# Kernel optimization log

Hardware: AMD Instinct MI355X
Metric: run time of the kernel (lower is better)

## Reference

```python
import jax, jax.numpy as jnp
import numpy as np

N_NODES = 100000
N_EDGES = 3200000
N_GRAPHS = 64
NEG_SLOPE = 0.2


def mish(x):
    return x * jnp.tanh(jax.nn.softplus(x))


def gat_layer(x, src, dst, W, b, a_src, a_dst, heads, out_ch, n_nodes):
    # h: [N, H, C]
    h = (x @ W).reshape(n_nodes, heads, out_ch)
    alpha_s = jnp.sum(h * a_src[None], axis=-1)  # [N, H]
    alpha_d = jnp.sum(h * a_dst[None], axis=-1)  # [N, H]
    e = jax.nn.leaky_relu(alpha_s[src] + alpha_d[dst], NEG_SLOPE)  # [E, H]
    # scatter-softmax over incoming edges of each destination node
    emax = jax.ops.segment_max(e, dst, num_segments=n_nodes)  # [N, H]
    ee = jnp.exp(e - emax[dst])
    den = jax.ops.segment_sum(ee, dst, num_segments=n_nodes)
    alpha = ee / (den[dst] + 1e-16)  # [E, H]
    msg = h[src] * alpha[..., None]  # [E, H, C]
    out = jax.ops.segment_sum(msg, dst, num_segments=n_nodes)
    return out.reshape(n_nodes, heads * out_ch) + b


def setup_inputs() -> dict:
    key = jax.random.key(0)
    ks = jax.random.split(key, 10)
    x = jax.random.normal(ks[0], (N_NODES, 128), dtype=jnp.float32)
    edge_index = jax.random.randint(ks[1], (2, N_EDGES), 0, N_NODES, dtype=jnp.int64)
    batch = jnp.sort(jax.random.randint(ks[2], (N_NODES,), 0, N_GRAPHS, dtype=jnp.int64))
    s1 = 1.0 / np.sqrt(128.0)
    s2 = 1.0 / np.sqrt(16.0)
    return {
        "x": x,
        "edge_index": edge_index,
        "batch": batch,
        "W1": jax.random.normal(ks[3], (128, 16), dtype=jnp.float32) * s1,
        "b1": jnp.zeros((16,), dtype=jnp.float32),
        "a_src1": jax.random.normal(ks[4], (4, 4), dtype=jnp.float32) * 0.5,
        "a_dst1": jax.random.normal(ks[5], (4, 4), dtype=jnp.float32) * 0.5,
        "W2": jax.random.normal(ks[6], (16, 32), dtype=jnp.float32) * s2,
        "b2": jnp.zeros((32,), dtype=jnp.float32),
        "a_src2": jax.random.normal(ks[7], (1, 32), dtype=jnp.float32) * 0.5,
        "a_dst2": jax.random.normal(ks[8], (1, 32), dtype=jnp.float32) * 0.5,
    }


def reference(x, edge_index, batch, W1, b1, a_src1, a_dst1, W2, b2, a_src2, a_dst2):
    n = x.shape[0]
    # PyG GATConv default add_self_loops=True
    loop = jnp.arange(n, dtype=edge_index.dtype)
    src = jnp.concatenate([edge_index[0], loop])
    dst = jnp.concatenate([edge_index[1], loop])
    h = mish(gat_layer(x, src, dst, W1, b1, a_src1, a_dst1, heads=4, out_ch=4, n_nodes=n))
    h = mish(gat_layer(h, src, dst, W2, b2, a_src2, a_dst2, heads=1, out_ch=32, n_nodes=n))
    # global_mean_pool
    sums = jax.ops.segment_sum(h, batch, num_segments=N_GRAPHS)
    cnts = jax.ops.segment_sum(jnp.ones((n,), h.dtype), batch, num_segments=N_GRAPHS)
    return sums / jnp.maximum(cnts, 1.0)[:, None]
```

## Files before the change

kernel.cpp:

```cpp
#include <hip/hip_runtime.h>
#include <hip/hip_fp16.h>
#include <math.h>

#define NEG_SLOPE 0.2f
#define GB 192
#define SB 320
#define CHMAX 11264
#define CAP 5120
#define CAPH 2560

typedef _Float16 half2v __attribute__((ext_vector_type(2)));
typedef _Float16 half4v __attribute__((ext_vector_type(4)));

__device__ __forceinline__ float mishf(float x) {
    if (x > 15.f) return x;
    float ex = __expf(x);
    float y = 1.f + ex;
    float y2 = y * y;
    return x * (y2 - 1.f) / (y2 + 1.f);
}

__device__ __forceinline__ float lw(float e) {
    return __expf(fmaxf(e, NEG_SLOPE * e));
}

__device__ __forceinline__ float hdot2a(half2v a, half2v b, float c) {
#if __has_builtin(__builtin_amdgcn_fdot2)
    return __builtin_amdgcn_fdot2(a, b, c, false);
#else
    return (float)a.x * (float)b.x + (float)a.y * (float)b.y + c;
#endif
}

__global__ __launch_bounds__(1024) void front_kernel(
        const float* __restrict__ x, const float* __restrict__ W1,
        const float* __restrict__ a_dst,
        const float* __restrict__ W2, const float* __restrict__ as2,
        const float* __restrict__ ad2,
        _Float16* __restrict__ hpre1h, float* __restrict__ addst,
        float* __restrict__ vs, float* __restrict__ vd,
        const int* __restrict__ src, const int* __restrict__ dst,
        int E, int Etot, int CH, int NB, int N, int NT,
        int* __restrict__ cursor, int* __restrict__ pairs) {
    __shared__ __attribute__((aligned(16))) char smem[63824];
    int tid = threadIdx.x;
    if (blockIdx.x < GB) {
        float* Wlt = (float*)smem;
        float* xs  = Wlt + 16 * 132;
        if (blockIdx.x == 0 && tid < 16) {
            float ps = 0.f, pd = 0.f;
            #pragma unroll
            for (int c = 0; c < 32; c++) {
                float w = W2[tid * 32 + c];
                ps += w * as2[c];
                pd += w * ad2[c];
            }
            vs[tid] = ps; vd[tid] = pd;
        }
        for (int i = tid; i < 2048; i += 1024) Wlt[(i & 15) * 132 + (i >> 4)] = W1[i];
        int nl = tid >> 4, ch = tid & 15;
        for (int t = blockIdx.x; t < NT; t += GB) {
            int nodebase = t * 64;
            int nvalid = min(64, N - nodebase);
            __syncthreads();
            const float4* x4 = (const float4*)(x + (size_t)nodebase * 128);
            #pragma unroll
            for (int u = 0; u < 2; u++) {
                int i = tid + (u << 10);
                int tnl = i >> 5;
                if (tnl < nvalid) {
                    float4 v = x4[i];
                    int k = (i & 31) * 4;
                    float* dp = &xs[tnl * 132 + k];
                    dp[0] = v.x; dp[1] = v.y; dp[2] = v.z; dp[3] = v.w;
                }
            }
            __syncthreads();
            if (nl < nvalid) {
                const float4* xr4 = (const float4*)&xs[nl * 132];
                const float4* wr4 = (const float4*)&Wlt[ch * 132];
                float acc = 0.f;
                #pragma unroll
                for (int k4 = 0; k4 < 32; k4++) {
                    float4 xv = xr4[k4];
                    float4 wv = wr4[k4];
                    acc += xv.x * wv.x + xv.y * wv.y + xv.z * wv.z + xv.w * wv.w;
                }
                int node = nodebase + nl;
                hpre1h[node * 16 + ch] = (_Float16)acc;
                float pd = acc * a_dst[ch];
                pd += __shfl_xor(pd, 1); pd += __shfl_xor(pd, 2);
                if ((ch & 3) == 0) addst[node * 4 + (ch >> 2)] = pd;
            }
        }
    } else {
        int nb2 = 2 * NB;
        int* A    = (int*)smem;
        int* Boff = A + nb2;
        int* C    = Boff + nb2;
        int* buf  = C + nb2;
        int blk = blockIdx.x - GB;
        for (int b = tid; b < nb2; b += 1024) A[b] = 0;
        __syncthreads();
        int ibeg = blk * CH, iend = min((blk + 1) * CH, Etot);
        int cdv[11], cs[11];
        #pragma unroll
        for (int u = 0; u < 11; u++) {
            int i = ibeg + tid + (u << 10);
            int d = -1, s = 0;
            if (i < iend) {
                if (i < E) { d = dst[i]; s = src[i]; } else { d = i - E; s = d; }
                atomicAdd(&A[d >> 6], 1);
            }
            cdv[u] = d; cs[u] = s;
        }
        for (int i = ibeg + CHMAX + tid; i < iend; i += 1024) {
            int d, s;
            if (i < E) { d = dst[i]; s = src[i]; } else { d = i - E; s = d; }
            int f = d >> 6;
            int pos = atomicAdd(&cursor[f], 1);
            pos = pos < CAPH ? pos : CAPH - 1;
            size_t addr = (size_t)(f >> 1) * CAP + ((f & 1) ? (CAP - 1 - pos) : pos);
            pairs[addr] = s | ((d & 63) << 17);
        }
        __syncthreads();
        for (int b = tid; b < nb2; b += 1024) Boff[b] = A[b];
        __syncthreads();
        for (int o = 1; o < nb2; o <<= 1) {
            int i1 = tid, i2 = tid + 1024;
            int v1 = 0, v2 = 0;
            if (i1 < nb2 && i1 >= o) v1 = Boff[i1 - o];
            if (i2 < nb2 && i2 >= o) v2 = Boff[i2 - o];
            __syncthreads();
            if (i1 < nb2) Boff[i1] += v1;
            if (i2 < nb2) Boff[i2] += v2;
            __syncthreads();
        }
        for (int b = tid; b < nb2; b += 1024) {
            int cnt = A[b];
            Boff[b] -= cnt;
            C[b] = cnt ? atomicAdd(&cursor[b], cnt) : 0;
        }
        __syncthreads();
        for (int b = tid; b < nb2; b += 1024) A[b] = 0;
        __syncthreads();
        #pragma unroll
        for (int u = 0; u < 11; u++) {
            int d = cdv[u];
            if (d < 0) continue;
            int f = d >> 6;
            int r = atomicAdd(&A[f], 1);
            buf[Boff[f] + r] = cs[u] | ((d & 63) << 17);
        }
        __syncthreads();
        int total = iend - ibeg;
        if (total > CHMAX) total = CHMAX;
        if (total < 0) total = 0;
        for (int j = tid; j < total; j += 1024) {
            int lo = 0, hi = nb2 - 1;
            while (lo < hi) {
                int mid = (lo + hi + 1) >> 1;
                if (Boff[mid] <= j) lo = mid; else hi = mid - 1;
            }
            int f = lo;
            int pos = C[f] + (j - Boff[f]);
            pos = pos < CAPH ? pos : CAPH - 1;
            size_t addr = (size_t)(f >> 1) * CAP + ((f & 1) ? (CAP - 1 - pos) : pos);
            pairs[addr] = buf[j];
        }
    }
}

__global__ __launch_bounds__(256) void csragg1_kernel(
        const int* __restrict__ pairs, const int* __restrict__ btotal,
        int NB, int N,
        int* __restrict__ ssorted, int* __restrict__ rs, int* __restrict__ re,
        const float* __restrict__ a_src1, const float* __restrict__ addst,
        const _Float16* __restrict__ hpre1h, const float* __restrict__ b1,
        const float* __restrict__ vs, const float* __restrict__ vd,
        _Float16* __restrict__ hpost1h,
        float* __restrict__ as2n, float* __restrict__ ad2n) {
    __shared__ int deg[64];
    __shared__ int s[64];
    __shared__ int cur[64];
    __shared__ __attribute__((aligned(16))) int lds_sorted[CAPH];
    int tid = threadIdx.x, bh = blockIdx.x;
    int B = bh >> 1, half = bh & 1;
    int nb0 = (B << 7) + (half << 6);
    int cnt_nodes = min(64, N - nb0);
    int c = min(btotal[bh], CAPH);
    int rbase = B * CAP + (half ? CAP - c : 0);
    if (tid < 64) deg[tid] = 0;
    __syncthreads();
    for (int j = tid; j < c; j += 256)
        atomicAdd(&deg[(pairs[rbase + j] >> 17) & 63], 1);
    __syncthreads();
    if (tid < 64) s[tid] = deg[tid];
    __syncthreads();
    for (int o = 1; o < 64; o <<= 1) {
        int v = 0;
        if (tid < 64 && tid >= o) v = s[tid - o];
        __syncthreads();
        if (tid < 64) s[tid] += v;
        __syncthreads();
    }
    if (tid < 64) {
        int ex = s[tid] - deg[tid];
        cur[tid] = ex;
        if (tid < cnt_nodes) {
            rs[nb0 + tid] = bh * CAPH + ex;
            re[nb0 + tid] = bh * CAPH + ex + deg[tid];
        }
    }
    __syncthreads();
    for (int j = tid; j < c; j += 256) {
        int p = pairs[rbase + j];
        int pos = atomicAdd(&cur[(p >> 17) & 63], 1);
        lds_sorted[pos < CAPH ? pos : CAPH - 1] = p & 0x1FFFF;
    }
    __syncthreads();

    {
        int t4 = c >> 2;
        const int4* ls4 = (const int4*)lds_sorted;
        int4* gs4 = (int4*)(ssorted + (size_t)bh * CAPH);
        for (int j = tid; j < t4; j += 256) gs4[j] = ls4[j];
        for (int j = (t4 << 2) + tid; j < c; j += 256)
            ssorted[(size_t)bh * CAPH + j] = lds_sorted[j];
    }

    int wave = tid >> 6;
    int lane = tid & 63;
    int head = lane & 3, er = lane >> 2;
    int c0 = head * 4;
    half2v w01, w23;
    w01.x = (_Float16)a_src1[c0];     w01.y = (_Float16)a_src1[c0 + 1];
    w23.x = (_Float16)a_src1[c0 + 2]; w23.y = (_Float16)a_src1[c0 + 3];
    for (int r = 0; r < 16; r++) {
        int ln = (wave << 4) + r;
        if (ln >= cnt_nodes) break;
        int node = nb0 + ln;
        int end = cur[ln];
        int start = end - deg[ln];
        float adh = addst[node * 4 + head];
        float den = 0.f, a0 = 0.f, a1 = 0.f, a2 = 0.f, a3 = 0.f;
        int last = end - 1;
        int jb = start;
        for (; jb + 16 <= end; jb += 16) {
            int s0 = lds_sorted[jb + er];
            half4v h = *(const half4v*)(hpre1h + (size_t)s0 * 16 + c0);
            half2v hlo = __builtin_shufflevector(h, h, 0, 1);
            half2v hhi = __builtin_shufflevector(h, h, 2, 3);
            float p = hdot2a(hlo, w01, hdot2a(hhi, w23, 0.f));
            float w = lw(p + adh);
            den += w;
            a0 += (float)h.x * w; a1 += (float)h.y * w;
            a2 += (float)h.z * w; a3 += (float)h.w * w;
        }
        if (jb < end) {
            int j0 = jb + er;
            int k0 = (j0 <= last) ? j0 : last;
            int s0 = lds_sorted[k0];
            half4v h = *(const half4v*)(hpre1h + (size_t)s0 * 16 + c0);
            half2v hlo = __builtin_shufflevector(h, h, 0, 1);
            half2v hhi = __builtin_shufflevector(h, h, 2, 3);
            float p = hdot2a(hlo, w01, hdot2a(hhi, w23, 0.f));
            float w = (j0 <= last) ? lw(p + adh) : 0.f;
            den += w;
            a0 += (float)h.x * w; a1 += (float)h.y * w;
            a2 += (float)h.z * w; a3 += (float)h.w * w;
        }
        a0 += __shfl_xor(a0, 4);  a1 += __shfl_xor(a1, 4);  a2 += __shfl_xor(a2, 4);  a3 += __shfl_xor(a3, 4);  den += __shfl_xor(den, 4);
        a0 += __shfl_xor(a0, 8);  a1 += __shfl_xor(a1, 8);  a2 += __shfl_xor(a2, 8);  a3 += __shfl_xor(a3, 8);  den += __shfl_xor(den, 8);
        a0 += __shfl_xor(a0, 16); a1 += __shfl_xor(a1, 16); a2 += __shfl_xor(a2, 16); a3 += __shfl_xor(a3, 16); den += __shfl_xor(den, 16);
        a0 += __shfl_xor(a0, 32); a1 += __shfl_xor(a1, 32); a2 += __shfl_xor(a2, 32); a3 += __shfl_xor(a3, 32); den += __shfl_xor(den, 32);
        if (er == 0) {
            float inv = 1.f / (den + 1e-16f);
            float o0 = mishf(a0 * inv + b1[c0]);
            float o1 = mishf(a1 * inv + b1[c0 + 1]);
            float o2 = mishf(a2 * inv + b1[c0 + 2]);
            float o3 = mishf(a3 * inv + b1[c0 + 3]);
            half4v oh;
            oh.x = (_Float16)o0; oh.y = (_Float16)o1;
            oh.z = (_Float16)o2; oh.w = (_Float16)o3;
            *(half4v*)(hpost1h + (size_t)node * 16 + c0) = oh;
            float ps = o0 * vs[c0] + o1 * vs[c0 + 1] + o2 * vs[c0 + 2] + o3 * vs[c0 + 3];
            float pd = o0 * vd[c0] + o1 * vd[c0 + 1] + o2 * vd[c0 + 2] + o3 * vd[c0 + 3];
            ps += __shfl_xor(ps, 1); pd += __shfl_xor(pd, 1);
            ps += __shfl_xor(ps, 2); pd += __shfl_xor(pd, 2);
            if (head == 0) { as2n[node] = ps; ad2n[node] = pd; }
        }
    }
}

__global__ void agg2_kernel(const int* __restrict__ rs, const int* __restrict__ re,
                            const int* __restrict__ ssorted,
                            const float* __restrict__ as2n, const float* __restrict__ ad2n,
                            const _Float16* __restrict__ hpost1h,
                            float* __restrict__ agg16, float* __restrict__ denv, int N) {
    int wave = threadIdx.x >> 6;
    int lane = threadIdx.x & 63;
    int node = blockIdx.x * 4 + wave;
    if (node >= N) return;
    int start = rs[node], end = re[node];
    int q = lane & 3, er = lane >> 2;
    int c0 = q * 4;
    float adh = ad2n[node];
    const _Float16* hb = hpost1h + c0;
    float den = 0.f, a0 = 0.f, a1 = 0.f, a2 = 0.f, a3 = 0.f;
    int last = end - 1;
    int jb = start;
    for (; jb + 16 <= end; jb += 16) {
        int s0 = __builtin_nontemporal_load(ssorted + jb + er);
        float w = lw(as2n[s0] + adh);
        half4v h = *(const half4v*)(hb + (size_t)s0 * 16);
        den += w;
        a0 += (float)h.x * w; a1 += (float)h.y * w;
        a2 += (float)h.z * w; a3 += (float)h.w * w;
    }
    if (jb < end) {
        int j0 = jb + er;
        int k0 = (j0 <= last) ? j0 : last;
        int s0 = __builtin_nontemporal_load(ssorted + k0);
        float w = (j0 <= last) ? lw(as2n[s0] + adh) : 0.f;
        half4v h = *(const half4v*)(hb + (size_t)s0 * 16);
        den += w;
        a0 += (float)h.x * w; a1 += (float)h.y * w;
        a2 += (float)h.z * w; a3 += (float)h.w * w;
    }
    a0 += __shfl_xor(a0, 4);  a1 += __shfl_xor(a1, 4);  a2 += __shfl_xor(a2, 4);  a3 += __shfl_xor(a3, 4);  den += __shfl_xor(den, 4);
    a0 += __shfl_xor(a0, 8);  a1 += __shfl_xor(a1, 8);  a2 += __shfl_xor(a2, 8);  a3 += __shfl_xor(a3, 8);  den += __shfl_xor(den, 8);
    a0 += __shfl_xor(a0, 16); a1 += __shfl_xor(a1, 16); a2 += __shfl_xor(a2, 16); a3 += __shfl_xor(a3, 16); den += __shfl_xor(den, 16);
    a0 += __shfl_xor(a0, 32); a1 += __shfl_xor(a1, 32); a2 += __shfl_xor(a2, 32); a3 += __shfl_xor(a3, 32); den += __shfl_xor(den, 32);
    if (er == 0) {
        float4 o; o.x = a0; o.y = a1; o.z = a2; o.w = a3;
        *(float4*)(agg16 + (size_t)node * 16 + c0) = o;
        if (q == 0) denv[node] = den;
    }
}

__global__ void post2pool_kernel(const float* __restrict__ agg16, const float* __restrict__ denv,
                                 const float* __restrict__ W2, const float* __restrict__ b2,
                                 const int* __restrict__ batch,
                                 float* __restrict__ pool, float* __restrict__ cnt, int N) {
    __shared__ float Wl[16 * 32];
    int tid = threadIdx.x;
    for (int i = tid; i < 512; i += 256) Wl[i] = W2[i];
    __syncthreads();
    int r = tid >> 5, ch = tid & 31;
    float bc = b2[ch];
    int base = blockIdx.x * 128;
    int cur = -1;
    float sum = 0.f, c = 0.f;
    for (int it = 0; it < 16; it++) {
        int n = base + it * 8 + r;
        if (n >= N) break;
        int g = batch[n];
        if (g != cur) {
            if (cur >= 0) {
                atomicAdd(&pool[cur * 32 + ch], sum);
                if (ch == 0) atomicAdd(&cnt[cur], c);
            }
            cur = g; sum = 0.f; c = 0.f;
        }
        const float* ar = agg16 + (size_t)n * 16;
        float acc = 0.f;
        #pragma unroll
        for (int k = 0; k < 16; k++) acc += ar[k] * Wl[k * 32 + ch];
        float val = mishf(acc / (denv[n] + 1e-16f) + bc);
        sum += val;
        c += 1.f;
    }
    if (cur >= 0) {
        atomicAdd(&pool[cur * 32 + ch], sum);
        if (ch == 0) atomicAdd(&cnt[cur], c);
    }
}

__global__ void fin_kernel(const float* __restrict__ pool, const float* __restrict__ cnt,
                           float* __restrict__ out, int NG) {
    int i = blockIdx.x * blockDim.x + threadIdx.x;
    if (i >= NG * 32) return;
    out[i] = pool[i] / fmaxf(cnt[i >> 5], 1.0f);
}

extern "C" void kernel_launch(void* const* d_in, const int* in_sizes, int n_in,
                              void* d_out, int out_size, void* d_ws, size_t ws_size,
                              hipStream_t stream) {
    const float* x   = (const float*)d_in[0];
    const int* eidx  = (const int*)d_in[1];
    const int* batch = (const int*)d_in[2];
    const float* W1  = (const float*)d_in[3];
    const float* b1  = (const float*)d_in[4];
    const float* as1 = (const float*)d_in[5];
    const float* ad1 = (const float*)d_in[6];
    const float* W2  = (const float*)d_in[7];
    const float* b2  = (const float*)d_in[8];
    const float* as2 = (const float*)d_in[9];
    const float* ad2 = (const float*)d_in[10];
    float* out = (float*)d_out;

    int N = in_sizes[0] / 128;
    int E = in_sizes[1] / 2;
    int Etot = E + N;
    int NG = out_size / 32;
    const int* esrc = eidx;
    const int* edst = eidx + E;

    int NB = (N + 127) >> 7;
    int NBH = NB * 2;
    int NT = (N + 63) >> 6;
    int CH = (Etot + SB - 1) / SB;

    char* p = (char*)d_ws;
    auto alloc = [&](size_t nbytes) {
        p = (char*)(((uintptr_t)p + 15) & ~(uintptr_t)15);
        void* r = (void*)p; p += nbytes; return r;
    };
    int* pairs        = (int*)alloc((size_t)NB * CAP * 4);
    int* ssorted      = (int*)alloc((size_t)NBH * CAPH * 4);
    int* rs           = (int*)alloc((size_t)N * 4);
    int* re           = (int*)alloc((size_t)N * 4);
    int* cursor       = (int*)alloc((size_t)NBH * 4);
    _Float16* hpre1h  = (_Float16*)alloc((size_t)N * 16 * 2);
    _Float16* hpost1h = (_Float16*)alloc((size_t)N * 16 * 2);
    float* addst1  = (float*)alloc((size_t)N * 4 * 4);
    float* as2n    = (float*)alloc((size_t)N * 4);
    float* ad2n    = (float*)alloc((size_t)N * 4);
    float* agg16   = (float*)alloc((size_t)N * 16 * 4);
    float* denv    = (float*)alloc((size_t)N * 4);
    float* vs      = (float*)alloc(16 * 4);
    float* vd      = (float*)alloc(16 * 4);
    float* pool    = (float*)alloc((size_t)NG * 32 * 4);
    float* cnt     = (float*)alloc((size_t)NG * 4);

    hipMemsetAsync(cursor, 0, (size_t)NBH * 4, stream);
    hipMemsetAsync(pool, 0, (size_t)NG * 32 * 4, stream);
    hipMemsetAsync(cnt, 0, (size_t)NG * 4, stream);

    front_kernel<<<GB + SB, 1024, 0, stream>>>(x, W1, ad1, W2, as2, ad2,
                                               hpre1h, addst1, vs, vd,
                                               esrc, edst, E, Etot, CH, NB, N, NT,
                                               cursor, pairs);
    csragg1_kernel<<<NBH, 256, 0, stream>>>(pairs, cursor, NB, N,
                                            ssorted, rs, re, as1, addst1, hpre1h,
                                            b1, vs, vd, hpost1h, as2n, ad2n);
    agg2_kernel<<<(N + 3) / 4, 256, 0, stream>>>(rs, re, ssorted, as2n, ad2n, hpost1h,
                                                 agg16, denv, N);
    post2pool_kernel<<<(N + 127) / 128, 256, 0, stream>>>(agg16, denv, W2, b2, batch,
                                                          pool, cnt, N);
    fin_kernel<<<(NG * 32 + 255) / 256, 256, 0, stream>>>(pool, cnt, out, NG);
}
```

Baseline: 332.9 us.

## Fuse CSR build, both aggregations and pooling into one cooperative kernel

Replaces the csragg1, agg2 and post2pool kernels with a single cooperative kernel. Each block handles two 64-node halves and keeps the sorted source lists in LDS across a grid-wide sync, so the ssorted/rs/re and agg16/denv global round trips and two launches disappear. Layer-2 aggregates stay in LDS for the pooling step. In exchange, each block now does twice the work sequentially, grid size drops to NB (about 782) blocks, LDS use per block grows (about 26 KB), which can limit occupancy. The cooperative launch also requires every block to be co-resident.

```diff
diff --git a/kernel.cpp b/kernel.cpp
--- a/kernel.cpp
+++ b/kernel.cpp
@@ -1,6 +1,9 @@
 #include <hip/hip_runtime.h>
 #include <hip/hip_fp16.h>
+#include <hip/hip_cooperative_groups.h>
 #include <math.h>
+
+namespace cg = cooperative_groups;
 
 #define NEG_SLOPE 0.2f
 #define GB 192
@@ -171,209 +174,201 @@
     }
 }
 
-__global__ __launch_bounds__(256) void csragg1_kernel(
-        const int* __restrict__ pairs, const int* __restrict__ btotal,
-        int NB, int N,
-        int* __restrict__ ssorted, int* __restrict__ rs, int* __restrict__ re,
+__global__ __launch_bounds__(256, 4) void mega_kernel(
+        const int* __restrict__ pairs, const int* __restrict__ cursor, int N,
         const float* __restrict__ a_src1, const float* __restrict__ addst,
         const _Float16* __restrict__ hpre1h, const float* __restrict__ b1,
         const float* __restrict__ vs, const float* __restrict__ vd,
         _Float16* __restrict__ hpost1h,
-        float* __restrict__ as2n, float* __restrict__ ad2n) {
-    __shared__ int deg[64];
-    __shared__ int s[64];
-    __shared__ int cur[64];
-    __shared__ __attribute__((aligned(16))) int lds_sorted[CAPH];
-    int tid = threadIdx.x, bh = blockIdx.x;
-    int B = bh >> 1, half = bh & 1;
-    int nb0 = (B << 7) + (half << 6);
-    int cnt_nodes = min(64, N - nb0);
-    int c = min(btotal[bh], CAPH);
-    int rbase = B * CAP + (half ? CAP - c : 0);
-    if (tid < 64) deg[tid] = 0;
-    __syncthreads();
-    for (int j = tid; j < c; j += 256)
-        atomicAdd(&deg[(pairs[rbase + j] >> 17) & 63], 1);
-    __syncthreads();
-    if (tid < 64) s[tid] = deg[tid];
-    __syncthreads();
-    for (int o = 1; o < 64; o <<= 1) {
-        int v = 0;
-        if (tid < 64 && tid >= o) v = s[tid - o];
-        __syncthreads();
-        if (tid < 64) s[tid] += v;
-        __syncthreads();
-    }
-    if (tid < 64) {
-        int ex = s[tid] - deg[tid];
-        cur[tid] = ex;
-        if (tid < cnt_nodes) {
-            rs[nb0 + tid] = bh * CAPH + ex;
-            re[nb0 + tid] = bh * CAPH + ex + deg[tid];
-        }
-    }
-    __syncthreads();
-    for (int j = tid; j < c; j += 256) {
-        int p = pairs[rbase + j];
-        int pos = atomicAdd(&cur[(p >> 17) & 63], 1);
-        lds_sorted[pos < CAPH ? pos : CAPH - 1] = p & 0x1FFFF;
-    }
-    __syncthreads();
-
-    {
-        int t4 = c >> 2;
-        const int4* ls4 = (const int4*)lds_sorted;
-        int4* gs4 = (int4*)(ssorted + (size_t)bh * CAPH);
-        for (int j = tid; j < t4; j += 256) gs4[j] = ls4[j];
-        for (int j = (t4 << 2) + tid; j < c; j += 256)
-            ssorted[(size_t)bh * CAPH + j] = lds_sorted[j];
-    }
+        float* __restrict__ as2n, float* __restrict__ ad2n,
+        const float* __restrict__ W2, const float* __restrict__ b2,
+        const int* __restrict__ batch,
+        float* __restrict__ pool, float* __restrict__ cntg) {
+    __shared__ __attribute__((aligned(16))) int lds_sorted[2][CAPH];
+    __shared__ int deg2[2][64];
+    __shared__ int cur2[2][64];
+    __shared__ int stmp[64];
+    __shared__ float W2l[512];
+    __shared__ float lds_agg[64 * 17];
+    __shared__ float lds_den[64];
+    int tid = threadIdx.x, blk = blockIdx.x;
+
+    for (int i = tid; i < 512; i += 256) W2l[i] = W2[i];
 
     int wave = tid >> 6;
     int lane = tid & 63;
-    int head = lane & 3, er = lane >> 2;
-    int c0 = head * 4;
-    half2v w01, w23;
-    w01.x = (_Float16)a_src1[c0];     w01.y = (_Float16)a_src1[c0 + 1];
-    w23.x = (_Float16)a_src1[c0 + 2]; w23.y = (_Float16)a_src1[c0 + 3];
-    for (int r = 0; r < 16; r++) {
-        int ln = (wave << 4) + r;
-        if (ln >= cnt_nodes) break;
-        int node = nb0 + ln;
-        int end = cur[ln];
-        int start = end - deg[ln];
-        float adh = addst[node * 4 + head];
-        float den = 0.f, a0 = 0.f, a1 = 0.f, a2 = 0.f, a3 = 0.f;
-        int last = end - 1;
-        int jb = start;
-        for (; jb + 16 <= end; jb += 16) {
-            int s0 = lds_sorted[jb + er];
-            half4v h = *(const half4v*)(hpre1h + (size_t)s0 * 16 + c0);
-            half2v hlo = __builtin_shufflevector(h, h, 0, 1);
-            half2v hhi = __builtin_shufflevector(h, h, 2, 3);
-            float p = hdot2a(hlo, w01, hdot2a(hhi, w23, 0.f));
-            float w = lw(p + adh);
-            den += w;
-            a0 += (float)h.x * w; a1 += (float)h.y * w;
-            a2 += (float)h.z * w; a3 += (float)h.w * w;
-        }
-        if (jb < end) {
-            int j0 = jb + er;
-            int k0 = (j0 <= last) ? j0 : last;
-            int s0 = lds_sorted[k0];
-            half4v h = *(const half4v*)(hpre1h + (size_t)s0 * 16 + c0);
-            half2v hlo = __builtin_shufflevector(h, h, 0, 1);
-            half2v hhi = __builtin_shufflevector(h, h, 2, 3);
-            float p = hdot2a(hlo, w01, hdot2a(hhi, w23, 0.f));
-            float w = (j0 <= last) ? lw(p + adh) : 0.f;
-            den += w;
-            a0 += (float)h.x * w; a1 += (float)h.y * w;
-            a2 += (float)h.z * w; a3 += (float)h.w * w;
-        }
-        a0 += __shfl_xor(a0, 4);  a1 += __shfl_xor(a1, 4);  a2 += __shfl_xor(a2, 4);  a3 += __shfl_xor(a3, 4);  den += __shfl_xor(den, 4);
-        a0 += __shfl_xor(a0, 8);  a1 += __shfl_xor(a1, 8);  a2 += __shfl_xor(a2, 8);  a3 += __shfl_xor(a3, 8);  den += __shfl_xor(den, 8);
-        a0 += __shfl_xor(a0, 16); a1 += __shfl_xor(a1, 16); a2 += __shfl_xor(a2, 16); a3 += __shfl_xor(a3, 16); den += __shfl_xor(den, 16);
-        a0 += __shfl_xor(a0, 32); a1 += __shfl_xor(a1, 32); a2 += __shfl_xor(a2, 32); a3 += __shfl_xor(a3, 32); den += __shfl_xor(den, 32);
-        if (er == 0) {
-            float inv = 1.f / (den + 1e-16f);
-            float o0 = mishf(a0 * inv + b1[c0]);
-            float o1 = mishf(a1 * inv + b1[c0 + 1]);
-            float o2 = mishf(a2 * inv + b1[c0 + 2]);
-            float o3 = mishf(a3 * inv + b1[c0 + 3]);
-            half4v oh;
-            oh.x = (_Float16)o0; oh.y = (_Float16)o1;
-            oh.z = (_Float16)o2; oh.w = (_Float16)o3;
-            *(half4v*)(hpost1h + (size_t)node * 16 + c0) = oh;
-            float ps = o0 * vs[c0] + o1 * vs[c0 + 1] + o2 * vs[c0 + 2] + o3 * vs[c0 + 3];
-            float pd = o0 * vd[c0] + o1 * vd[c0 + 1] + o2 * vd[c0 + 2] + o3 * vd[c0 + 3];
-            ps += __shfl_xor(ps, 1); pd += __shfl_xor(pd, 1);
-            ps += __shfl_xor(ps, 2); pd += __shfl_xor(pd, 2);
-            if (head == 0) { as2n[node] = ps; ad2n[node] = pd; }
-        }
+
+    for (int half = 0; half < 2; half++) {
+        int f = (blk << 1) | half;
+        int nb0 = (blk << 7) + (half << 6);
+        int cnt_nodes = min(64, N - nb0);
+        int c = min(cursor[f], CAPH);
+        int rbase = blk * CAP + (half ? CAP - c : 0);
+        if (tid < 64) deg2[half][tid] = 0;
+        __syncthreads();
+        for (int j = tid; j < c; j += 256)
+            atomicAdd(&deg2[half][(pairs[rbase + j] >> 17) & 63], 1);
+        __syncthreads();
+        if (tid < 64) stmp[tid] = deg2[half][tid];
+        __syncthreads();
+        for (int o = 1; o < 64; o <<= 1) {
+            int v = 0;
+            if (tid < 64 && tid >= o) v = stmp[tid - o];
+            __syncthreads();
+            if (tid < 64) stmp[tid] += v;
+            __syncthreads();
+        }
+        if (tid < 64) cur2[half][tid] = stmp[tid] - deg2[half][tid];
+        __syncthreads();
+        for (int j = tid; j < c; j += 256) {
+            int p = pairs[rbase + j];
+            int pos = atomicAdd(&cur2[half][(p >> 17) & 63], 1);
+            lds_sorted[half][pos < CAPH ? pos : CAPH - 1] = p & 0x1FFFF;
+        }
+        __syncthreads();
+
+        int head = lane & 3, er = lane >> 2;
+        int c0 = head * 4;
+        half2v w01, w23;
+        w01.x = (_Float16)a_src1[c0];     w01.y = (_Float16)a_src1[c0 + 1];
+        w23.x = (_Float16)a_src1[c0 + 2]; w23.y = (_Float16)a_src1[c0 + 3];
+        for (int r = 0; r < 16; r++) {
+            int ln = (wave << 4) + r;
+            if (ln >= cnt_nodes) break;
+            int node = nb0 + ln;
+            int end = cur2[half][ln];
+            int start = end - deg2[half][ln];
+            float adh = addst[node * 4 + head];
+            float den = 0.f, a0 = 0.f, a1 = 0.f, a2 = 0.f, a3 = 0.f;
+            int last = end - 1;
+            int jb = start;
+            for (; jb + 16 <= end; jb += 16) {
+                int s0 = lds_sorted[half][jb + er];
+                half4v h = *(const half4v*)(hpre1h + (size_t)s0 * 16 + c0);
+                half2v hlo = __builtin_shufflevector(h, h, 0, 1);
+                half2v hhi = __builtin_shufflevector(h, h, 2, 3);
+                float p = hdot2a(hlo, w01, hdot2a(hhi, w23, 0.f));
+                float w = lw(p + adh);
+                den += w;
+                a0 += (float)h.x * w; a1 += (float)h.y * w;
+                a2 += (float)h.z * w; a3 += (float)h.w * w;
+            }
+            if (jb < end) {
+                int j0 = jb + er;
+                int k0 = (j0 <= last) ? j0 : last;
+                int s0 = lds_sorted[half][k0];
+                half4v h = *(const half4v*)(hpre1h + (size_t)s0 * 16 + c0);
+                half2v hlo = __builtin_shufflevector(h, h, 0, 1);
+                half2v hhi = __builtin_shufflevector(h, h, 2, 3);
+                float p = hdot2a(hlo, w01, hdot2a(hhi, w23, 0.f));
+                float w = (j0 <= last) ? lw(p + adh) : 0.f;
+                den += w;
+                a0 += (float)h.x * w; a1 += (float)h.y * w;
+                a2 += (float)h.z * w; a3 += (float)h.w * w;
+            }
+            a0 += __shfl_xor(a0, 4);  a1 += __shfl_xor(a1, 4);  a2 += __shfl_xor(a2, 4);  a3 += __shfl_xor(a3, 4);  den += __shfl_xor(den, 4);
+            a0 += __shfl_xor(a0, 8);  a1 += __shfl_xor(a1, 8);  a2 += __shfl_xor(a2, 8);  a3 += __shfl_xor(a3, 8);  den += __shfl_xor(den, 8);
+            a0 += __shfl_xor(a0, 16); a1 += __shfl_xor(a1, 16); a2 += __shfl_xor(a2, 16); a3 += __shfl_xor(a3, 16); den += __shfl_xor(den, 16);
+            a0 += __shfl_xor(a0, 32); a1 += __shfl_xor(a1, 32); a2 += __shfl_xor(a2, 32); a3 += __shfl_xor(a3, 32); den += __shfl_xor(den, 32);
+            if (er == 0) {
+                float inv = 1.f / (den + 1e-16f);
+                float o0 = mishf(a0 * inv + b1[c0]);
+                float o1 = mishf(a1 * inv + b1[c0 + 1]);
+                float o2 = mishf(a2 * inv + b1[c0 + 2]);
+                float o3 = mishf(a3 * inv + b1[c0 + 3]);
+                half4v oh;
+                oh.x = (_Float16)o0; oh.y = (_Float16)o1;
+                oh.z = (_Float16)o2; oh.w = (_Float16)o3;
+                *(half4v*)(hpost1h + (size_t)node * 16 + c0) = oh;
+                float ps = o0 * vs[c0] + o1 * vs[c0 + 1] + o2 * vs[c0 + 2] + o3 * vs[c0 + 3];
+                float pd = o0 * vd[c0] + o1 * vd[c0 + 1] + o2 * vd[c0 + 2] + o3 * vd[c0 + 3];
+                ps += __shfl_xor(ps, 1); pd += __shfl_xor(pd, 1);
+                ps += __shfl_xor(ps, 2); pd += __shfl_xor(pd, 2);
+                if (head == 0) { as2n[node] = ps; ad2n[node] = pd; }
+            }
+        }
+        __syncthreads();
     }
-}
-
-__global__ void agg2_kernel(const int* __restrict__ rs, const int* __restrict__ re,
-                            const int* __restrict__ ssorted,
-                            const float* __restrict__ as2n, const float* __restrict__ ad2n,
-                            const _Float16* __restrict__ hpost1h,
-                            float* __restrict__ agg16, float* __restrict__ denv, int N) {
-    int wave = threadIdx.x >> 6;
-    int lane = threadIdx.x & 63;
-    int node = blockIdx.x * 4 + wave;
-    if (node >= N) return;
-    int start = rs[node], end = re[node];
-    int q = lane & 3, er = lane >> 2;
-    int c0 = q * 4;
-    float adh = ad2n[node];
-    const _Float16* hb = hpost1h + c0;
-    float den = 0.f, a0 = 0.f, a1 = 0.f, a2 = 0.f, a3 = 0.f;
-    int last = end - 1;
-    int jb = start;
-    for (; jb + 16 <= end; jb += 16) {
-        int s0 = __builtin_nontemporal_load(ssorted + jb + er);
-        float w = lw(as2n[s0] + adh);
-        half4v h = *(const half4v*)(hb + (size_t)s0 * 16);
-        den += w;
-        a0 += (float)h.x * w; a1 += (float)h.y * w;
-        a2 += (float)h.z * w; a3 += (float)h.w * w;
-    }
-    if (jb < end) {
-        int j0 = jb + er;
-        int k0 = (j0 <= last) ? j0 : last;
-        int s0 = __builtin_nontemporal_load(ssorted + k0);
-        float w = (j0 <= last) ? lw(as2n[s0] + adh) : 0.f;
-        half4v h = *(const half4v*)(hb + (size_t)s0 * 16);
-        den += w;
-        a0 += (float)h.x * w; a1 += (float)h.y * w;
-        a2 += (float)h.z * w; a3 += (float)h.w * w;
-    }
-    a0 += __shfl_xor(a0, 4);  a1 += __shfl_xor(a1, 4);  a2 += __shfl_xor(a2, 4);  a3 += __shfl_xor(a3, 4);  den += __shfl_xor(den, 4);
-    a0 += __shfl_xor(a0, 8);  a1 += __shfl_xor(a1, 8);  a2 += __shfl_xor(a2, 8);  a3 += __shfl_xor(a3, 8);  den += __shfl_xor(den, 8);
-    a0 += __shfl_xor(a0, 16); a1 += __shfl_xor(a1, 16); a2 += __shfl_xor(a2, 16); a3 += __shfl_xor(a3, 16); den += __shfl_xor(den, 16);
-    a0 += __shfl_xor(a0, 32); a1 += __shfl_xor(a1, 32); a2 += __shfl_xor(a2, 32); a3 += __shfl_xor(a3, 32); den += __shfl_xor(den, 32);
-    if (er == 0) {
-        float4 o; o.x = a0; o.y = a1; o.z = a2; o.w = a3;
-        *(float4*)(agg16 + (size_t)node * 16 + c0) = o;
-        if (q == 0) denv[node] = den;
-    }
-}
-
-__global__ void post2pool_kernel(const float* __restrict__ agg16, const float* __restrict__ denv,
-                                 const float* __restrict__ W2, const float* __restrict__ b2,
-                                 const int* __restrict__ batch,
-                                 float* __restrict__ pool, float* __restrict__ cnt, int N) {
-    __shared__ float Wl[16 * 32];
-    int tid = threadIdx.x;
-    for (int i = tid; i < 512; i += 256) Wl[i] = W2[i];
-    __syncthreads();
-    int r = tid >> 5, ch = tid & 31;
-    float bc = b2[ch];
-    int base = blockIdx.x * 128;
-    int cur = -1;
-    float sum = 0.f, c = 0.f;
-    for (int it = 0; it < 16; it++) {
-        int n = base + it * 8 + r;
-        if (n >= N) break;
-        int g = batch[n];
-        if (g != cur) {
-            if (cur >= 0) {
-                atomicAdd(&pool[cur * 32 + ch], sum);
-                if (ch == 0) atomicAdd(&cnt[cur], c);
-            }
-            cur = g; sum = 0.f; c = 0.f;
-        }
-        const float* ar = agg16 + (size_t)n * 16;
-        float acc = 0.f;
-        #pragma unroll
-        for (int k = 0; k < 16; k++) acc += ar[k] * Wl[k * 32 + ch];
-        float val = mishf(acc / (denv[n] + 1e-16f) + bc);
-        sum += val;
-        c += 1.f;
-    }
-    if (cur >= 0) {
-        atomicAdd(&pool[cur * 32 + ch], sum);
-        if (ch == 0) atomicAdd(&cnt[cur], c);
+
+    __threadfence();
+    cg::this_grid().sync();
+
+    for (int half = 0; half < 2; half++) {
+        int nb0 = (blk << 7) + (half << 6);
+        int cnt_nodes = min(64, N - nb0);
+
+        int q = lane & 3, er = lane >> 2;
+        int c0 = q * 4;
+        const _Float16* hb = hpost1h + c0;
+        for (int r = 0; r < 16; r++) {
+            int ln = (wave << 4) + r;
+            if (ln >= cnt_nodes) break;
+            int node = nb0 + ln;
+            int end = cur2[half][ln];
+            int start = end - deg2[half][ln];
+            float adh = ad2n[node];
+            float den = 0.f, a0 = 0.f, a1 = 0.f, a2 = 0.f, a3 = 0.f;
+            int last = end - 1;
+            int jb = start;
+            for (; jb + 16 <= end; jb += 16) {
+                int s0 = lds_sorted[half][jb + er];
+                float w = lw(as2n[s0] + adh);
+                half4v h = *(const half4v*)(hb + (size_t)s0 * 16);
+                den += w;
+                a0 += (float)h.x * w; a1 += (float)h.y * w;
+                a2 += (float)h.z * w; a3 += (float)h.w * w;
+            }
+            if (jb < end) {
+                int j0 = jb + er;
+                int k0 = (j0 <= last) ? j0 : last;
+                int s0 = lds_sorted[half][k0];
+                float w = (j0 <= last) ? lw(as2n[s0] + adh) : 0.f;
+                half4v h = *(const half4v*)(hb + (size_t)s0 * 16);
+                den += w;
+                a0 += (float)h.x * w; a1 += (float)h.y * w;
+                a2 += (float)h.z * w; a3 += (float)h.w * w;
+            }
+            a0 += __shfl_xor(a0, 4);  a1 += __shfl_xor(a1, 4);  a2 += __shfl_xor(a2, 4);  a3 += __shfl_xor(a3, 4);  den += __shfl_xor(den, 4);
+            a0 += __shfl_xor(a0, 8);  a1 += __shfl_xor(a1, 8);  a2 += __shfl_xor(a2, 8);  a3 += __shfl_xor(a3, 8);  den += __shfl_xor(den, 8);
+            a0 += __shfl_xor(a0, 16); a1 += __shfl_xor(a1, 16); a2 += __shfl_xor(a2, 16); a3 += __shfl_xor(a3, 16); den += __shfl_xor(den, 16);
+            a0 += __shfl_xor(a0, 32); a1 += __shfl_xor(a1, 32); a2 += __shfl_xor(a2, 32); a3 += __shfl_xor(a3, 32); den += __shfl_xor(den, 32);
+            if (er == 0) {
+                float* ag = &lds_agg[ln * 17 + c0];
+                ag[0] = a0; ag[1] = a1; ag[2] = a2; ag[3] = a3;
+                if (q == 0) lds_den[ln] = den;
+            }
+        }
+        __syncthreads();
+
+        int rr = tid >> 5, ch = tid & 31;
+        float bc = b2[ch];
+        int curg = -1;
+        float sum = 0.f, cc = 0.f;
+        for (int it = 0; it < 8; it++) {
+            int ln = it * 8 + rr;
+            if (ln >= cnt_nodes) break;
+            int n = nb0 + ln;
+            int g = batch[n];
+            if (g != curg) {
+                if (curg >= 0) {
+                    atomicAdd(&pool[curg * 32 + ch], sum);
+                    if (ch == 0) atomicAdd(&cntg[curg], cc);
+                }
+                curg = g; sum = 0.f; cc = 0.f;
+            }
+            const float* ar = &lds_agg[ln * 17];
+            float acc = 0.f;
+            #pragma unroll
+            for (int k = 0; k < 16; k++) acc += ar[k] * W2l[k * 32 + ch];
+            float val = mishf(acc / (lds_den[ln] + 1e-16f) + bc);
+            sum += val;
+            cc += 1.f;
+        }
+        if (curg >= 0) {
+            atomicAdd(&pool[curg * 32 + ch], sum);
+            if (ch == 0) atomicAdd(&cntg[curg], cc);
+        }
+        __syncthreads();
     }
 }
 
@@ -418,17 +413,12 @@
         void* r = (void*)p; p += nbytes; return r;
     };
     int* pairs        = (int*)alloc((size_t)NB * CAP * 4);
-    int* ssorted      = (int*)alloc((size_t)NBH * CAPH * 4);
-    int* rs           = (int*)alloc((size_t)N * 4);
-    int* re           = (int*)alloc((size_t)N * 4);
     int* cursor       = (int*)alloc((size_t)NBH * 4);
     _Float16* hpre1h  = (_Float16*)alloc((size_t)N * 16 * 2);
     _Float16* hpost1h = (_Float16*)alloc((size_t)N * 16 * 2);
     float* addst1  = (float*)alloc((size_t)N * 4 * 4);
     float* as2n    = (float*)alloc((size_t)N * 4);
     float* ad2n    = (float*)alloc((size_t)N * 4);
-    float* agg16   = (float*)alloc((size_t)N * 16 * 4);
-    float* denv    = (float*)alloc((size_t)N * 4);
     float* vs      = (float*)alloc(16 * 4);
     float* vd      = (float*)alloc(16 * 4);
     float* pool    = (float*)alloc((size_t)NG * 32 * 4);
@@ -442,12 +432,14 @@
                                                hpre1h, addst1, vs, vd,
                                                esrc, edst, E, Etot, CH, NB, N, NT,
                                                cursor, pairs);
-    csragg1_kernel<<<NBH, 256, 0, stream>>>(pairs, cursor, NB, N,
-                                            ssorted, rs, re, as1, addst1, hpre1h,
-                                            b1, vs, vd, hpost1h, as2n, ad2n);
-    agg2_kernel<<<(N + 3) / 4, 256, 0, stream>>>(rs, re, ssorted, as2n, ad2n, hpost1h,
-                                                 agg16, denv, N);
-    post2pool_kernel<<<(N + 127) / 128, 256, 0, stream>>>(agg16, denv, W2, b2, batch,
-                                                          pool, cnt, N);
+
+    void* margs[] = {(void*)&pairs, (void*)&cursor, (void*)&N,
+                     (void*)&as1, (void*)&addst1, (void*)&hpre1h, (void*)&b1,
+                     (void*)&vs, (void*)&vd, (void*)&hpost1h,
+                     (void*)&as2n, (void*)&ad2n, (void*)&W2, (void*)&b2,
+                     (void*)&batch, (void*)&pool, (void*)&cnt};
+    hipLaunchCooperativeKernel((void*)mega_kernel, dim3(NB), dim3(256),
+                               margs, 0, stream);
+
     fin_kernel<<<(NG * 32 + 255) / 256, 256, 0, stream>>>(pool, cnt, out, NG);
 }
```

Result: slower. 555.4 us (+66.8%).

## Pack layer-2 features with source scores, unroll gathers, remap agg2 blocks per XCD

Applied to the files above, without the earlier changes.

Stores each node's layer-1 output (16 halves) together with its layer-2 source attention score in a single 64-byte record, so the agg2 gather fetches the weight and the features from one cache line instead of two separate arrays. Both aggregation loops now process two edges per lane per iteration, which puts more independent gathers in flight. agg2 block indices are remapped so that consecutive 64-node groups are spread across the 8 XCDs. The cost is a larger record (32 bytes per node of padding) and a larger tail overhead for low-degree nodes.

```diff
diff --git a/kernel.cpp b/kernel.cpp
--- a/kernel.cpp
+++ b/kernel.cpp
@@ -178,8 +178,8 @@
         const float* __restrict__ a_src1, const float* __restrict__ addst,
         const _Float16* __restrict__ hpre1h, const float* __restrict__ b1,
         const float* __restrict__ vs, const float* __restrict__ vd,
-        _Float16* __restrict__ hpost1h,
-        float* __restrict__ as2n, float* __restrict__ ad2n) {
+        _Float16* __restrict__ hpack,
+        float* __restrict__ ad2n) {
     __shared__ int deg[64];
     __shared__ int s[64];
     __shared__ int cur[64];
@@ -246,29 +246,46 @@
         float den = 0.f, a0 = 0.f, a1 = 0.f, a2 = 0.f, a3 = 0.f;
         int last = end - 1;
         int jb = start;
-        for (; jb + 16 <= end; jb += 16) {
+        for (; jb + 32 <= end; jb += 32) {
             int s0 = lds_sorted[jb + er];
-            half4v h = *(const half4v*)(hpre1h + (size_t)s0 * 16 + c0);
-            half2v hlo = __builtin_shufflevector(h, h, 0, 1);
-            half2v hhi = __builtin_shufflevector(h, h, 2, 3);
-            float p = hdot2a(hlo, w01, hdot2a(hhi, w23, 0.f));
-            float w = lw(p + adh);
-            den += w;
-            a0 += (float)h.x * w; a1 += (float)h.y * w;
-            a2 += (float)h.z * w; a3 += (float)h.w * w;
+            int s1 = lds_sorted[jb + 16 + er];
+            half4v h0 = *(const half4v*)(hpre1h + (size_t)s0 * 16 + c0);
+            half4v h1 = *(const half4v*)(hpre1h + (size_t)s1 * 16 + c0);
+            half2v h0lo = __builtin_shufflevector(h0, h0, 0, 1);
+            half2v h0hi = __builtin_shufflevector(h0, h0, 2, 3);
+            half2v h1lo = __builtin_shufflevector(h1, h1, 0, 1);
+            half2v h1hi = __builtin_shufflevector(h1, h1, 2, 3);
+            float p0 = hdot2a(h0lo, w01, hdot2a(h0hi, w23, 0.f));
+            float p1 = hdot2a(h1lo, w01, hdot2a(h1hi, w23, 0.f));
+            float wt0 = lw(p0 + adh);
+            float wt1 = lw(p1 + adh);
+            den += wt0 + wt1;
+            a0 += (float)h0.x * wt0 + (float)h1.x * wt1;
+            a1 += (float)h0.y * wt0 + (float)h1.y * wt1;
+            a2 += (float)h0.z * wt0 + (float)h1.z * wt1;
+            a3 += (float)h0.w * wt0 + (float)h1.w * wt1;
         }
         if (jb < end) {
-            int j0 = jb + er;
+            int j0 = jb + er, j1 = jb + 16 + er;
             int k0 = (j0 <= last) ? j0 : last;
+            int k1 = (j1 <= last) ? j1 : last;
             int s0 = lds_sorted[k0];
-            half4v h = *(const half4v*)(hpre1h + (size_t)s0 * 16 + c0);
-            half2v hlo = __builtin_shufflevector(h, h, 0, 1);
-            half2v hhi = __builtin_shufflevector(h, h, 2, 3);
-            float p = hdot2a(hlo, w01, hdot2a(hhi, w23, 0.f));
-            float w = (j0 <= last) ? lw(p + adh) : 0.f;
-            den += w;
-            a0 += (float)h.x * w; a1 += (float)h.y * w;
-            a2 += (float)h.z * w; a3 += (float)h.w * w;
+            int s1 = lds_sorted[k1];
+            half4v h0 = *(const half4v*)(hpre1h + (size_t)s0 * 16 + c0);
+            half4v h1 = *(const half4v*)(hpre1h + (size_t)s1 * 16 + c0);
+            half2v h0lo = __builtin_shufflevector(h0, h0, 0, 1);
+            half2v h0hi = __builtin_shufflevector(h0, h0, 2, 3);
+            half2v h1lo = __builtin_shufflevector(h1, h1, 0, 1);
+            half2v h1hi = __builtin_shufflevector(h1, h1, 2, 3);
+            float p0 = hdot2a(h0lo, w01, hdot2a(h0hi, w23, 0.f));
+            float p1 = hdot2a(h1lo, w01, hdot2a(h1hi, w23, 0.f));
+            float wt0 = (j0 <= last) ? lw(p0 + adh) : 0.f;
+            float wt1 = (j1 <= last) ? lw(p1 + adh) : 0.f;
+            den += wt0 + wt1;
+            a0 += (float)h0.x * wt0 + (float)h1.x * wt1;
+            a1 += (float)h0.y * wt0 + (float)h1.y * wt1;
+            a2 += (float)h0.z * wt0 + (float)h1.z * wt1;
+            a3 += (float)h0.w * wt0 + (float)h1.w * wt1;
         }
         a0 += __shfl_xor(a0, 4);  a1 += __shfl_xor(a1, 4);  a2 += __shfl_xor(a2, 4);  a3 += __shfl_xor(a3, 4);  den += __shfl_xor(den, 4);
         a0 += __shfl_xor(a0, 8);  a1 += __shfl_xor(a1, 8);  a2 += __shfl_xor(a2, 8);  a3 += __shfl_xor(a3, 8);  den += __shfl_xor(den, 8);
@@ -283,50 +300,76 @@
             half4v oh;
             oh.x = (_Float16)o0; oh.y = (_Float16)o1;
             oh.z = (_Float16)o2; oh.w = (_Float16)o3;
-            *(half4v*)(hpost1h + (size_t)node * 16 + c0) = oh;
+            _Float16* rec = hpack + (size_t)node * 32;
+            *(half4v*)(rec + c0) = oh;
             float ps = o0 * vs[c0] + o1 * vs[c0 + 1] + o2 * vs[c0 + 2] + o3 * vs[c0 + 3];
             float pd = o0 * vd[c0] + o1 * vd[c0 + 1] + o2 * vd[c0 + 2] + o3 * vd[c0 + 3];
             ps += __shfl_xor(ps, 1); pd += __shfl_xor(pd, 1);
             ps += __shfl_xor(ps, 2); pd += __shfl_xor(pd, 2);
-            if (head == 0) { as2n[node] = ps; ad2n[node] = pd; }
+            if (head == 0) {
+                *(float*)(rec + 16) = ps;
+                ad2n[node] = pd;
+            }
         }
     }
 }
 
 __global__ void agg2_kernel(const int* __restrict__ rs, const int* __restrict__ re,
                             const int* __restrict__ ssorted,
-                            const float* __restrict__ as2n, const float* __restrict__ ad2n,
-                            const _Float16* __restrict__ hpost1h,
+                            const _Float16* __restrict__ hpack,
+                            const float* __restrict__ ad2n,
                             float* __restrict__ agg16, float* __restrict__ denv, int N) {
     int wave = threadIdx.x >> 6;
     int lane = threadIdx.x & 63;
-    int node = blockIdx.x * 4 + wave;
+    int b = blockIdx.x;
+    int xcd = b & 7, i = b >> 3;
+    int f = xcd + ((i >> 4) << 3);
+    int sub = i & 15;
+    int node = f * 64 + sub * 4 + wave;
     if (node >= N) return;
     int start = rs[node], end = re[node];
     int q = lane & 3, er = lane >> 2;
     int c0 = q * 4;
     float adh = ad2n[node];
-    const _Float16* hb = hpost1h + c0;
     float den = 0.f, a0 = 0.f, a1 = 0.f, a2 = 0.f, a3 = 0.f;
     int last = end - 1;
     int jb = start;
-    for (; jb + 16 <= end; jb += 16) {
+    for (; jb + 32 <= end; jb += 32) {
         int s0 = __builtin_nontemporal_load(ssorted + jb + er);
-        float w = lw(as2n[s0] + adh);
-        half4v h = *(const half4v*)(hb + (size_t)s0 * 16);
-        den += w;
-        a0 += (float)h.x * w; a1 += (float)h.y * w;
-        a2 += (float)h.z * w; a3 += (float)h.w * w;
+        int s1 = __builtin_nontemporal_load(ssorted + jb + 16 + er);
+        const _Float16* r0 = hpack + (size_t)s0 * 32;
+        const _Float16* r1 = hpack + (size_t)s1 * 32;
+        float as0 = *(const float*)(r0 + 16);
+        float as1 = *(const float*)(r1 + 16);
+        half4v h0 = *(const half4v*)(r0 + c0);
+        half4v h1 = *(const half4v*)(r1 + c0);
+        float wt0 = lw(as0 + adh);
+        float wt1 = lw(as1 + adh);
+        den += wt0 + wt1;
+        a0 += (float)h0.x * wt0 + (float)h1.x * wt1;
+        a1 += (float)h0.y * wt0 + (float)h1.y * wt1;
+        a2 += (float)h0.z * wt0 + (float)h1.z * wt1;
+        a3 += (float)h0.w * wt0 + (float)h1.w * wt1;
     }
     if (jb < end) {
-        int j0 = jb + er;
+        int j0 = jb + er, j1 = jb + 16 + er;
         int k0 = (j0 <= last) ? j0 : last;
+        int k1 = (j1 <= last) ? j1 : last;
         int s0 = __builtin_nontemporal_load(ssorted + k0);
-        float w = (j0 <= last) ? lw(as2n[s0] + adh) : 0.f;
-        half4v h = *(const half4v*)(hb + (size_t)s0 * 16);
-        den += w;
-        a0 += (float)h.x * w; a1 += (float)h.y * w;
-        a2 += (float)h.z * w; a3 += (float)h.w * w;
+        int s1 = __builtin_nontemporal_load(ssorted + k1);
+        const _Float16* r0 = hpack + (size_t)s0 * 32;
+        const _Float16* r1 = hpack + (size_t)s1 * 32;
+        float as0 = *(const float*)(r0 + 16);
+        float as1 = *(const float*)(r1 + 16);
+        half4v h0 = *(const half4v*)(r0 + c0);
+        half4v h1 = *(const half4v*)(r1 + c0);
+        float wt0 = (j0 <= last) ? lw(as0 + adh) : 0.f;
+        float wt1 = (j1 <= last) ? lw(as1 + adh) : 0.f;
+        den += wt0 + wt1;
+        a0 += (float)h0.x * wt0 + (float)h1.x * wt1;
+        a1 += (float)h0.y * wt0 + (float)h1.y * wt1;
+        a2 += (float)h0.z * wt0 + (float)h1.z * wt1;
+        a3 += (float)h0.w * wt0 + (float)h1.w * wt1;
     }
     a0 += __shfl_xor(a0, 4);  a1 += __shfl_xor(a1, 4);  a2 += __shfl_xor(a2, 4);  a3 += __shfl_xor(a3, 4);  den += __shfl_xor(den, 4);
     a0 += __shfl_xor(a0, 8);  a1 += __shfl_xor(a1, 8);  a2 += __shfl_xor(a2, 8);  a3 += __shfl_xor(a3, 8);  den += __shfl_xor(den, 8);
@@ -423,9 +466,8 @@
     int* re           = (int*)alloc((size_t)N * 4);
     int* cursor       = (int*)alloc((size_t)NBH * 4);
     _Float16* hpre1h  = (_Float16*)alloc((size_t)N * 16 * 2);
-    _Float16* hpost1h = (_Float16*)alloc((size_t)N * 16 * 2);
+    _Float16* hpack   = (_Float16*)alloc((size_t)N * 64);
     float* addst1  = (float*)alloc((size_t)N * 4 * 4);
-    float* as2n    = (float*)alloc((size_t)N * 4);
     float* ad2n    = (float*)alloc((size_t)N * 4);
     float* agg16   = (float*)alloc((size_t)N * 16 * 4);
     float* denv    = (float*)alloc((size_t)N * 4);
@@ -444,9 +486,10 @@
                                                cursor, pairs);
     csragg1_kernel<<<NBH, 256, 0, stream>>>(pairs, cursor, NB, N,
                                             ssorted, rs, re, as1, addst1, hpre1h,
-                                            b1, vs, vd, hpost1h, as2n, ad2n);
-    agg2_kernel<<<(N + 3) / 4, 256, 0, stream>>>(rs, re, ssorted, as2n, ad2n, hpost1h,
-                                                 agg16, denv, N);
+                                            b1, vs, vd, hpack, ad2n);
+    int NF = ((NBH + 7) >> 3) << 3;
+    agg2_kernel<<<NF * 16, 256, 0, stream>>>(rs, re, ssorted, hpack, ad2n,
+                                             agg16, denv, N);
     post2pool_kernel<<<(N + 127) / 128, 256, 0, stream>>>(agg16, denv, W2, b2, batch,
                                                           pool, cnt, N);
     fin_kernel<<<(NG * 32 + 255) / 256, 256, 0, stream>>>(pool, cnt, out, NG);
```

New measurement: 334.6 us. No clear change (+0.5%).
